# Performance work log

Measured on AMD Instinct MI355X. Metric: run time of the kernel, lower is better.

## Reference

```python
import jax, jax.numpy as jnp
import numpy as np

THETA = 0.5

def _l2norm(x):
    return x / jnp.maximum(jnp.linalg.norm(x, axis=-1, keepdims=True), 1e-12)

def _gcn_conv(x, row, col, W, b, n):
    # PyG GCNConv: add self loops (weight 1), sym-normalize, aggregate at col
    loop = jnp.arange(n)
    r = jnp.concatenate([row, loop])
    c = jnp.concatenate([col, loop])
    w = jnp.ones(r.shape[0], x.dtype)
    deg = jax.ops.segment_sum(w, c, num_segments=n)
    dinv = jnp.where(deg > 0, deg ** -0.5, 0.0)
    norm = dinv[r] * w * dinv[c]          # [E+N]
    xw = x @ W                            # [N, out]
    out = jax.ops.segment_sum(norm[:, None] * xw[r], c, num_segments=n)
    return out + b


def setup_inputs() -> dict:
    key = jax.random.key(0)
    ks = jax.random.split(key, 10)
    N, E, F, H, C = 16384, 524288, 256, 256, 40
    return {
        "edge_index": jax.random.randint(ks[0], (2, E), 0, N),
        "neg_edge_index": jax.random.randint(ks[1], (2, E), 0, N),
        "features": jax.random.normal(ks[2], (N, F), jnp.float32),
        "sim": jax.random.uniform(ks[3], (N, N), jnp.float32),
        "label_smoothing": jnp.ones((1,), jnp.float32),
        "W1": jax.random.normal(ks[4], (F, H), jnp.float32) * 0.05,
        "b1": jnp.zeros((H,), jnp.float32),
        "W2": jax.random.normal(ks[5], (H, H), jnp.float32) * 0.05,
        "b2": jnp.zeros((H,), jnp.float32),
        "Wy": jax.random.normal(ks[6], (H, C), jnp.float32) * 0.05,
        "by": jnp.zeros((C,), jnp.float32),
    }


def reference(edge_index, neg_edge_index, features, sim, label_smoothing,
              W1, b1, W2, b2, Wy, by):
    n = features.shape[0]
    row, col = edge_index[0], edge_index[1]
    # GCN encoder (dropout p=0.0 -> identity), L2-normalized twice as in source
    h = jax.nn.relu(_gcn_conv(features, row, col, W1, b1, n))
    h = _gcn_conv(h, row, col, W2, b2, n)
    rep = _l2norm(_l2norm(h))
    y = rep @ Wy + by
    # reconstruction loss; the i<j filtering becomes masking (jit-safe)
    pmask = (row < col).astype(rep.dtype)
    nr, nc = neg_edge_index[0], neg_edge_index[1]
    nmask = (nr < nc).astype(rep.dtype)
    neg_w = jax.nn.relu(jnp.sum(rep[nr] * rep[nc], axis=1))
    pos_w = jax.nn.relu(jnp.sum(rep[row] * rep[col], axis=1))
    pos_fsim = sim[row, col]
    pos = pos_fsim * THETA + pos_w * (1.0 - THETA)
    tgt = label_smoothing[0]
    sse = jnp.sum(nmask * neg_w ** 2) + jnp.sum(pmask * (pos - tgt) ** 2)
    rec_loss = sse * n / (jnp.sum(nmask) + jnp.sum(pmask))
    return rep, rec_loss, y
```

## Files before the change

kernel.cpp:

```cpp
#include <hip/hip_runtime.h>
#include <math.h>

typedef __attribute__((ext_vector_type(8))) short bf16x8;
typedef __attribute__((ext_vector_type(4))) float f32x4;
typedef __attribute__((ext_vector_type(2))) float f32x2;

static inline size_t align256(size_t x) { return (x + 255) & ~(size_t)255; }

__device__ inline ushort f2bf(float f) {
    uint u = __float_as_uint(f);
    u = (u + 0x7fffu + ((u >> 16) & 1u)) >> 16;
    return (ushort)u;
}
__device__ inline float bf2f(ushort b) { return __uint_as_float(((uint)b) << 16); }

__device__ inline uint f2fp8(float x) {
    float ax = fabsf(x);
    uint s = (__float_as_uint(x) >> 31) << 7;
    if (ax < 0.015625f) {
        int q = (int)rintf(ax * 512.f);
        if (q == 8) return s | 0x08u;
        return s | (uint)q;
    }
    uint u = __float_as_uint(ax);
    u += 0x7ffffu + ((u >> 20) & 1u);
    int e8 = (int)(u >> 23) - 127;
    uint m = (u >> 20) & 7u;
    return s | ((uint)(e8 + 7) << 3) | m;
}

#if __has_builtin(__builtin_amdgcn_cvt_pk_f32_fp8)
__device__ inline float fp8dot16(uint4 qa, uint4 qb) {
    uint ua[4] = {qa.x, qa.y, qa.z, qa.w};
    uint ub[4] = {qb.x, qb.y, qb.z, qb.w};
    float s = 0.f;
    #pragma unroll
    for (int i = 0; i < 4; i++) {
        f32x2 a0 = __builtin_amdgcn_cvt_pk_f32_fp8(ua[i], false);
        f32x2 a1 = __builtin_amdgcn_cvt_pk_f32_fp8(ua[i], true);
        f32x2 b0 = __builtin_amdgcn_cvt_pk_f32_fp8(ub[i], false);
        f32x2 b1 = __builtin_amdgcn_cvt_pk_f32_fp8(ub[i], true);
        s += a0.x * b0.x + a0.y * b0.y + a1.x * b1.x + a1.y * b1.y;
    }
    return s;
}
#else
__device__ inline float fp8dec(uint b) {
    uint s = (b >> 7) & 1u, e = (b >> 3) & 0xfu, m = b & 7u;
    float dn = (float)(int)m * 0.001953125f;
    float nf = __uint_as_float((s << 31) | ((e + 120u) << 23) | (m << 20));
    float dv = s ? -dn : dn;
    return e ? nf : dv;
}
__device__ inline float fp8dot16(uint4 qa, uint4 qb) {
    uint ua[4] = {qa.x, qa.y, qa.z, qa.w};
    uint ub[4] = {qb.x, qb.y, qb.z, qb.w};
    float s = 0.f;
    #pragma unroll
    for (int i = 0; i < 4; i++)
        #pragma unroll
        for (int j = 0; j < 4; j++)
            s += fp8dec((ua[i] >> (8 * j)) & 0xffu) * fp8dec((ub[i] >> (8 * j)) & 0xffu);
    return s;
}
#endif

__device__ inline void fma8(float* acc, uint4 q, float s) {
    acc[0] += s * bf2f((ushort)(q.x & 0xffff)); acc[1] += s * bf2f((ushort)(q.x >> 16));
    acc[2] += s * bf2f((ushort)(q.y & 0xffff)); acc[3] += s * bf2f((ushort)(q.y >> 16));
    acc[4] += s * bf2f((ushort)(q.z & 0xffff)); acc[5] += s * bf2f((ushort)(q.z >> 16));
    acc[6] += s * bf2f((ushort)(q.w & 0xffff)); acc[7] += s * bf2f((ushort)(q.w >> 16));
}

__global__ void prep_kernel(const int* __restrict__ e_col, int E, int* __restrict__ cnt,
                            const float* __restrict__ W1, const float* __restrict__ W2,
                            const float* __restrict__ Wy,
                            ushort* __restrict__ W1t, ushort* __restrict__ W2t,
                            ushort* __restrict__ WyTb, int H, int* __restrict__ ticket,
                            const int* __restrict__ pos_e, const float* __restrict__ sim,
                            float* __restrict__ simv, int N) {
    int i = blockIdx.x * blockDim.x + threadIdx.x;
    int HH = H * H;
    if (i == 0) *ticket = 0;
    if (i < E) {
        atomicAdd(&cnt[e_col[i]], 1);
    } else if (i < E + HH) {
        int j = i - E; int k = j / H, n = j % H;
        W1t[(size_t)n * H + k] = f2bf(W1[j]);
    } else if (i < E + 2 * HH) {
        int j = i - E - HH; int k = j / H, n = j % H;
        W2t[(size_t)n * H + k] = f2bf(W2[j]);
    } else if (i < E + 2 * HH + 64 * H) {
        int j = i - E - 2 * HH; int n = j / H, k = j % H;
        WyTb[j] = (n < 40) ? f2bf(Wy[(size_t)k * 40 + n]) : (ushort)0;
    } else if (i < E + 2 * HH + 64 * H + E) {
        int ei = i - (E + 2 * HH + 64 * H);
        int a = pos_e[ei], b = pos_e[E + ei];
        if (a < b) simv[ei] = sim[(size_t)a * N + b];
    }
}

__global__ __launch_bounds__(1024) void scan_offsets(const int* __restrict__ cnt,
                                                     int* __restrict__ offsets,
                                                     int* __restrict__ fillpos,
                                                     float* __restrict__ dinv, int N) {
    __shared__ int wsum[16];
    int t = threadIdx.x;
    int lane = t & 63, w = t >> 6;
    int i0 = t * 16;
    int cl[16];
    #pragma unroll
    for (int j = 0; j < 4; j++) {
        int4 c = *(const int4*)(cnt + i0 + j * 4);
        cl[j * 4 + 0] = c.x; cl[j * 4 + 1] = c.y; cl[j * 4 + 2] = c.z; cl[j * 4 + 3] = c.w;
    }
    int s = 0;
    #pragma unroll
    for (int j = 0; j < 16; j++) s += cl[j];
    int x = s;
    #pragma unroll
    for (int o = 1; o < 64; o <<= 1) { int y = __shfl_up(x, o); if (lane >= o) x += y; }
    if (lane == 63) wsum[w] = x;
    __syncthreads();
    if (w == 0 && lane < 16) {
        int v = wsum[lane];
        #pragma unroll
        for (int o = 1; o < 16; o <<= 1) { int y = __shfl_up(v, o); if (lane >= o) v += y; }
        wsum[lane] = v;
    }
    __syncthreads();
    int wbase = (w == 0) ? 0 : wsum[w - 1];
    int off = wbase + x - s;
    #pragma unroll
    for (int j = 0; j < 16; j++) {
        int i = i0 + j;
        offsets[i] = off;
        fillpos[i] = off;
        dinv[i] = rsqrtf((float)(cl[j] + 1));
        off += cl[j];
    }
    if (t == 1023) offsets[N] = off;
}

__global__ void fill_csr(const int* __restrict__ row, const int* __restrict__ col, int E,
                         int* __restrict__ fillpos, int* __restrict__ csr_src) {
    int e = blockIdx.x * blockDim.x + threadIdx.x;
    if (e < E) {
        int p = atomicAdd(&fillpos[col[e]], 1);
        csr_src[p] = row[e];
    }
}

template<bool AF32>
__global__ __launch_bounds__(256) void gemm_bf16_kernel(const void* __restrict__ Av,
                                                        const ushort* __restrict__ Bt,
                                                        ushort* __restrict__ C, int M) {
    __shared__ ushort As[128][40];
    __shared__ ushort Bs[128][40];
    const int K = 256;
    int t = threadIdx.x;
    int lane = t & 63, w = t >> 6;
    int wm = w >> 1, wn = w & 1;
    int brow = blockIdx.y * 128, bcol = blockIdx.x * 128;
    int l15 = lane & 15, l4 = lane >> 4;

    f32x4 acc[4][4];
    for (int i = 0; i < 4; i++)
        for (int j = 0; j < 4; j++) {
            f32x4 z = {0.f, 0.f, 0.f, 0.f};
            acc[i][j] = z;
        }

    for (int k0 = 0; k0 < K; k0 += 32) {
        #pragma unroll
        for (int i = 0; i < 2; i++) {
            int idx = t + i * 256;
            int r = idx >> 2, seg = idx & 3;
            if constexpr (AF32) {
                const float* A = (const float*)Av;
                const float* ap = A + (size_t)(brow + r) * K + k0 + seg * 8;
                float4 f0 = *(const float4*)ap;
                float4 f1 = *(const float4*)(ap + 4);
                uint4 va;
                va.x = f2bf(f0.x) | ((uint)f2bf(f0.y) << 16);
                va.y = f2bf(f0.z) | ((uint)f2bf(f0.w) << 16);
                va.z = f2bf(f1.x) | ((uint)f2bf(f1.y) << 16);
                va.w = f2bf(f1.z) | ((uint)f2bf(f1.w) << 16);
                *(uint4*)&As[r][seg * 8] = va;
            } else {
                const ushort* A = (const ushort*)Av;
                *(uint4*)&As[r][seg * 8] = *(const uint4*)(A + (size_t)(brow + r) * K + k0 + seg * 8);
            }
            *(uint4*)&Bs[r][seg * 8] = *(const uint4*)(Bt + (size_t)(bcol + r) * K + k0 + seg * 8);
        }
        __syncthreads();

        bf16x8 af[4], bfr[4];
        #pragma unroll
        for (int mf = 0; mf < 4; mf++)
            af[mf] = *(const bf16x8*)&As[wm * 64 + mf * 16 + l15][l4 * 8];
        #pragma unroll
        for (int nf = 0; nf < 4; nf++)
            bfr[nf] = *(const bf16x8*)&Bs[wn * 64 + nf * 16 + l15][l4 * 8];

        #pragma unroll
        for (int mf = 0; mf < 4; mf++)
            #pragma unroll
            for (int nf = 0; nf < 4; nf++)
                acc[mf][nf] = __builtin_amdgcn_mfma_f32_16x16x32_bf16(af[mf], bfr[nf], acc[mf][nf], 0, 0, 0);
        __syncthreads();
    }

    #pragma unroll
    for (int mf = 0; mf < 4; mf++)
        #pragma unroll
        for (int nf = 0; nf < 4; nf++)
            #pragma unroll
            for (int j = 0; j < 4; j++) {
                int r = brow + wm * 64 + mf * 16 + l4 * 4 + j;
                int c = bcol + wn * 64 + nf * 16 + l15;
                C[(size_t)r * 256 + c] = f2bf(acc[mf][nf][j]);
            }
}

__global__ __launch_bounds__(256) void gcn_agg1_kernel(const ushort* __restrict__ xw,
                                                       const float* __restrict__ dinv,
                                                       const int* __restrict__ offsets,
                                                       const int* __restrict__ csr_src,
                                                       const float* __restrict__ bias,
                                                       ushort* __restrict__ out_b, int N) {
    int t = threadIdx.x;
    int v = (blockIdx.x * blockDim.x + t) >> 5;
    int l = t & 31;
    if (v >= N) return;
    float dv = dinv[v];
    float acc[8] = {0, 0, 0, 0, 0, 0, 0, 0};
    uint4 q = *(const uint4*)(xw + (size_t)v * 256 + l * 8);
    fma8(acc, q, dv * dv);
    int beg = offsets[v], end = offsets[v + 1];
    int e = beg;
    for (; e + 4 <= end; e += 4) {
        int r0 = csr_src[e], r1 = csr_src[e + 1], r2 = csr_src[e + 2], r3 = csr_src[e + 3];
        float n0 = dinv[r0] * dv, n1 = dinv[r1] * dv, n2 = dinv[r2] * dv, n3 = dinv[r3] * dv;
        uint4 p0 = *(const uint4*)(xw + (size_t)r0 * 256 + l * 8);
        uint4 p1 = *(const uint4*)(xw + (size_t)r1 * 256 + l * 8);
        uint4 p2 = *(const uint4*)(xw + (size_t)r2 * 256 + l * 8);
        uint4 p3 = *(const uint4*)(xw + (size_t)r3 * 256 + l * 8);
        fma8(acc, p0, n0); fma8(acc, p1, n1); fma8(acc, p2, n2); fma8(acc, p3, n3);
    }
    for (; e < end; e++) {
        int r0 = csr_src[e];
        uint4 p0 = *(const uint4*)(xw + (size_t)r0 * 256 + l * 8);
        fma8(acc, p0, dinv[r0] * dv);
    }
    float4 b0 = *(const float4*)(bias + l * 8);
    float4 b1 = *(const float4*)(bias + l * 8 + 4);
    acc[0] = fmaxf(acc[0] + b0.x, 0.f); acc[1] = fmaxf(acc[1] + b0.y, 0.f);
    acc[2] = fmaxf(acc[2] + b0.z, 0.f); acc[3] = fmaxf(acc[3] + b0.w, 0.f);
    acc[4] = fmaxf(acc[4] + b1.x, 0.f); acc[5] = fmaxf(acc[5] + b1.y, 0.f);
    acc[6] = fmaxf(acc[6] + b1.z, 0.f); acc[7] = fmaxf(acc[7] + b1.w, 0.f);
    uint4 o;
    o.x = f2bf(acc[0]) | ((uint)f2bf(acc[1]) << 16);
    o.y = f2bf(acc[2]) | ((uint)f2bf(acc[3]) << 16);
    o.z = f2bf(acc[4]) | ((uint)f2bf(acc[5]) << 16);
    o.w = f2bf(acc[6]) | ((uint)f2bf(acc[7]) << 16);
    *(uint4*)(out_b + (size_t)v * 256 + l * 8) = o;
}

__global__ __launch_bounds__(256) void gcn_agg2_kernel(const ushort* __restrict__ xw,
                                                       const float* __restrict__ dinv,
                                                       const int* __restrict__ offsets,
                                                       const int* __restrict__ csr_src,
                                                       const float* __restrict__ b2,
                                                       float* __restrict__ rep,
                                                       ushort* __restrict__ repb,
                                                       unsigned char* __restrict__ rep8, int N) {
    int t = threadIdx.x;
    int v = (blockIdx.x * blockDim.x + t) >> 5;
    int l = t & 31;
    if (v >= N) return;
    float dv = dinv[v];
    float acc[8] = {0, 0, 0, 0, 0, 0, 0, 0};
    uint4 q = *(const uint4*)(xw + (size_t)v * 256 + l * 8);
    fma8(acc, q, dv * dv);
    int beg = offsets[v], end = offsets[v + 1];
    int e = beg;
    for (; e + 4 <= end; e += 4) {
        int r0 = csr_src[e], r1 = csr_src[e + 1], r2 = csr_src[e + 2], r3 = csr_src[e + 3];
        float n0 = dinv[r0] * dv, n1 = dinv[r1] * dv, n2 = dinv[r2] * dv, n3 = dinv[r3] * dv;
        uint4 p0 = *(const uint4*)(xw + (size_t)r0 * 256 + l * 8);
        uint4 p1 = *(const uint4*)(xw + (size_t)r1 * 256 + l * 8);
        uint4 p2 = *(const uint4*)(xw + (size_t)r2 * 256 + l * 8);
        uint4 p3 = *(const uint4*)(xw + (size_t)r3 * 256 + l * 8);
        fma8(acc, p0, n0); fma8(acc, p1, n1); fma8(acc, p2, n2); fma8(acc, p3, n3);
    }
    for (; e < end; e++) {
        int r0 = csr_src[e];
        uint4 p0 = *(const uint4*)(xw + (size_t)r0 * 256 + l * 8);
        fma8(acc, p0, dinv[r0] * dv);
    }
    float4 b0 = *(const float4*)(b2 + l * 8);
    float4 b1 = *(const float4*)(b2 + l * 8 + 4);
    acc[0] += b0.x; acc[1] += b0.y; acc[2] += b0.z; acc[3] += b0.w;
    acc[4] += b1.x; acc[5] += b1.y; acc[6] += b1.z; acc[7] += b1.w;

    float ss = 0.f;
    #pragma unroll
    for (int i = 0; i < 8; i++) ss += acc[i] * acc[i];
    #pragma unroll
    for (int o = 1; o < 32; o <<= 1) ss += __shfl_xor(ss, o);
    float n1 = fmaxf(sqrtf(ss), 1e-12f);
    float i1 = 1.f / n1;
    float n2 = fmaxf(sqrtf(ss) * i1, 1e-12f);
    float sc = i1 / n2;
    #pragma unroll
    for (int i = 0; i < 8; i++) acc[i] *= sc;

    float4 o0, o1;
    o0.x = acc[0]; o0.y = acc[1]; o0.z = acc[2]; o0.w = acc[3];
    o1.x = acc[4]; o1.y = acc[5]; o1.z = acc[6]; o1.w = acc[7];
    *(float4*)(rep + (size_t)v * 256 + l * 8) = o0;
    *(float4*)(rep + (size_t)v * 256 + l * 8 + 4) = o1;
    uint4 ob;
    ob.x = f2bf(acc[0]) | ((uint)f2bf(acc[1]) << 16);
    ob.y = f2bf(acc[2]) | ((uint)f2bf(acc[3]) << 16);
    ob.z = f2bf(acc[4]) | ((uint)f2bf(acc[5]) << 16);
    ob.w = f2bf(acc[6]) | ((uint)f2bf(acc[7]) << 16);
    *(uint4*)(repb + (size_t)v * 256 + l * 8) = ob;
    uint2 o8;
    o8.x = f2fp8(acc[0]) | (f2fp8(acc[1]) << 8) | (f2fp8(acc[2]) << 16) | (f2fp8(acc[3]) << 24);
    o8.y = f2fp8(acc[4]) | (f2fp8(acc[5]) << 8) | (f2fp8(acc[6]) << 16) | (f2fp8(acc[7]) << 24);
    *(uint2*)(rep8 + (size_t)v * 256 + l * 8) = o8;
}

__global__ __launch_bounds__(256) void tail_kernel(const ushort* __restrict__ repb,
                                                   const ushort* __restrict__ WyTb,
                                                   const float* __restrict__ by,
                                                   float* __restrict__ y,
                                                   const unsigned char* __restrict__ rep8,
                                                   const int* __restrict__ pos_e,
                                                   const int* __restrict__ neg_e,
                                                   const float* __restrict__ simv,
                                                   const float* __restrict__ lsm,
                                                   float2* __restrict__ partials,
                                                   int* __restrict__ ticket,
                                                   float* __restrict__ out_loss,
                                                   int E, int N, int NYB, int LB) {
    __shared__ ushort As[64][40];
    __shared__ ushort Bs[64][40];
    __shared__ float s_red[8];
    __shared__ int isLast;
    int t = threadIdx.x;

    if ((int)blockIdx.x < NYB) {
        const int K = 256;
        int lane = t & 63, w = t >> 6;
        int brow = blockIdx.x * 64;
        int l15 = lane & 15, l4 = lane >> 4;
        f32x4 acc[4];
        for (int i = 0; i < 4; i++) { f32x4 z = {0.f, 0.f, 0.f, 0.f}; acc[i] = z; }
        for (int k0 = 0; k0 < K; k0 += 32) {
            int r = t >> 2, seg = t & 3;
            *(uint4*)&As[r][seg * 8] = *(const uint4*)(repb + (size_t)(brow + r) * K + k0 + seg * 8);
            *(uint4*)&Bs[r][seg * 8] = *(const uint4*)(WyTb + (size_t)r * K + k0 + seg * 8);
            __syncthreads();
            bf16x8 af = *(const bf16x8*)&As[w * 16 + l15][l4 * 8];
            #pragma unroll
            for (int nf = 0; nf < 4; nf++) {
                bf16x8 bfr = *(const bf16x8*)&Bs[nf * 16 + l15][l4 * 8];
                acc[nf] = __builtin_amdgcn_mfma_f32_16x16x32_bf16(af, bfr, acc[nf], 0, 0, 0);
            }
            __syncthreads();
        }
        #pragma unroll
        for (int nf = 0; nf < 4; nf++)
            #pragma unroll
            for (int j = 0; j < 4; j++) {
                int r = brow + w * 16 + l4 * 4 + j;
                int c = nf * 16 + l15;
                if (c < 40) y[(size_t)r * 40 + c] = acc[nf][j] + by[c];
            }
        return;
    }

    int lb = (int)blockIdx.x - NYB;
    int l16 = t & 15;
    int g = lb * 16 + (t >> 4);
    int ng = LB * 16;
    float tgt = lsm[0];
    float sse = 0.f, cntf = 0.f;
    for (int idx = g; idx < 2 * E; idx += ng) {
        bool is_pos = idx < E;
        int ei = is_pos ? idx : idx - E;
        const int* ep = is_pos ? pos_e : neg_e;
        int a = ep[ei];
        int b = ep[E + ei];
        if (a < b) {
            uint4 qa = *(const uint4*)(rep8 + (size_t)a * 256 + l16 * 16);
            uint4 qb = *(const uint4*)(rep8 + (size_t)b * 256 + l16 * 16);
            float d = fp8dot16(qa, qb);
            #pragma unroll
            for (int o = 1; o < 16; o <<= 1) d += __shfl_xor(d, o);
            float wr = fmaxf(d, 0.f);
            float term;
            if (is_pos) {
                float fsim = simv[ei];
                float p = fsim * 0.5f + wr * 0.5f;
                term = (p - tgt) * (p - tgt);
            } else {
                term = wr * wr;
            }
            sse += term;
            cntf += 1.f;
        }
    }
    sse += __shfl_xor(sse, 16); cntf += __shfl_xor(cntf, 16);
    sse += __shfl_xor(sse, 32); cntf += __shfl_xor(cntf, 32);
    if ((t & 63) == 0) { s_red[t >> 6] = sse; s_red[4 + (t >> 6)] = cntf; }
    __syncthreads();
    if (t == 0) {
        float2 pp;
        pp.x = s_red[0] + s_red[1] + s_red[2] + s_red[3];
        pp.y = s_red[4] + s_red[5] + s_red[6] + s_red[7];
        partials[lb] = pp;
        __threadfence();
        int prev = atomicAdd(ticket, 1);
        isLast = (prev == LB - 1) ? 1 : 0;
    }
    __syncthreads();
    if (isLast) {
        __threadfence();
        float fs = 0.f, fc = 0.f;
        for (int i = t; i < LB; i += 256) {
            float2 pp = partials[i];
            fs += pp.x; fc += pp.y;
        }
        #pragma unroll
        for (int o = 1; o < 64; o <<= 1) { fs += __shfl_xor(fs, o); fc += __shfl_xor(fc, o); }
        if ((t & 63) == 0) { s_red[t >> 6] = fs; s_red[4 + (t >> 6)] = fc; }
        __syncthreads();
        if (t == 0) {
            float S = s_red[0] + s_red[1] + s_red[2] + s_red[3];
            float Cc = s_red[4] + s_red[5] + s_red[6] + s_red[7];
            out_loss[0] = S * (float)N / Cc;
        }
    }
}

extern "C" void kernel_launch(void* const* d_in, const int* in_sizes, int n_in,
                              void* d_out, int out_size, void* d_ws, size_t ws_size,
                              hipStream_t stream) {
    const int*   edge  = (const int*)d_in[0];
    const int*   nedge = (const int*)d_in[1];
    const float* feat  = (const float*)d_in[2];
    const float* sim   = (const float*)d_in[3];
    const float* lsm   = (const float*)d_in[4];
    const float* W1    = (const float*)d_in[5];
    const float* b1    = (const float*)d_in[6];
    const float* W2    = (const float*)d_in[7];
    const float* b2    = (const float*)d_in[8];
    const float* Wy    = (const float*)d_in[9];
    const float* by    = (const float*)d_in[10];

    const int E = in_sizes[0] / 2;
    const int H = in_sizes[6];
    const int F = in_sizes[5] / H;
    const int N = in_sizes[2] / F;

    const int* e_row = edge;
    const int* e_col = edge + E;

    const int LOSS_BLOCKS = 2048;
    const int NYB = N / 64;

    char* p = (char*)d_ws;
    int*    cnt      = (int*)p;    p += align256((size_t)N * 4);
    float*  dinv     = (float*)p;  p += align256((size_t)N * 4);
    int*    offsets  = (int*)p;    p += align256((size_t)(N + 1) * 4);
    int*    fillpos  = (int*)p;    p += align256((size_t)N * 4);
    int*    csr_src  = (int*)p;    p += align256((size_t)E * 4);
    ushort* W1t      = (ushort*)p; p += align256((size_t)F * H * 2);
    ushort* W2t      = (ushort*)p; p += align256((size_t)H * H * 2);
    ushort* WyTb     = (ushort*)p; p += align256((size_t)64 * H * 2);
    ushort* h1b      = (ushort*)p; p += align256((size_t)N * H * 2);
    ushort* xwb      = (ushort*)p; p += align256((size_t)N * H * 2);
    ushort* repb     = (ushort*)p; p += align256((size_t)N * H * 2);
    unsigned char* rep8 = (unsigned char*)p; p += align256((size_t)N * H);
    float*  simv     = (float*)p;  p += align256((size_t)E * 4);
    float2* partials = (float2*)p; p += align256((size_t)LOSS_BLOCKS * 8);
    int*    ticket   = (int*)p;    p += 256;

    float* rep  = (float*)d_out;
    float* loss = rep + (size_t)N * H;
    float* yout = loss + 1;

    hipMemsetAsync(cnt, 0, (size_t)N * 4, stream);

    {
        int total = 2 * E + 2 * H * H + 64 * H;
        prep_kernel<<<(total + 255) / 256, 256, 0, stream>>>(e_col, E, cnt, W1, W2, Wy,
                                                             W1t, W2t, WyTb, H, ticket,
                                                             e_row, sim, simv, N);
    }
    scan_offsets<<<1, 1024, 0, stream>>>(cnt, offsets, fillpos, dinv, N);
    fill_csr<<<(E + 255) / 256, 256, 0, stream>>>(e_row, e_col, E, fillpos, csr_src);

    {
        dim3 grid(2, N / 128);
        gemm_bf16_kernel<true><<<grid, 256, 0, stream>>>((const void*)feat, W1t, xwb, N);
    }
    gcn_agg1_kernel<<<N * 32 / 256, 256, 0, stream>>>(xwb, dinv, offsets, csr_src, b1, h1b, N);

    {
        dim3 grid(2, N / 128);
        gemm_bf16_kernel<false><<<grid, 256, 0, stream>>>((const void*)h1b, W2t, xwb, N);
    }
    gcn_agg2_kernel<<<N * 32 / 256, 256, 0, stream>>>(xwb, dinv, offsets, csr_src, b2,
                                                      rep, repb, rep8, N);

    tail_kernel<<<NYB + LOSS_BLOCKS, 256, 0, stream>>>(repb, WyTb, by, yout, rep8,
                                                       edge, nedge, simv, lsm, partials,
                                                       ticket, loss, E, N, NYB, LOSS_BLOCKS);
}
```

Measured before the change: 275.5 us.

## Fuse CSR fill with GEMM1, aggregation with GEMM2, and aggregation2 with y-projection

The CSR fill now runs as extra blocks inside the first GEMM launch. The first aggregation writes its bf16 output into shared memory and feeds the W2 GEMM directly, so the h1 buffer no longer makes a global round trip. The second aggregation likewise keeps normalized rep in shared memory and computes y = rep@Wy in the same block, and the loss becomes its own kernel. This removes launches and intermediate global traffic. The cost is fewer blocks in the aggregation kernels (N/64, each handling 64 nodes serially in 8 passes), which lowers parallelism and latency hiding for the gathers, plus larger LDS use.

```diff
diff --git a/kernel.cpp b/kernel.cpp
--- a/kernel.cpp
+++ b/kernel.cpp
@@ -142,59 +142,54 @@
     if (t == 1023) offsets[N] = off;
 }
 
-__global__ void fill_csr(const int* __restrict__ row, const int* __restrict__ col, int E,
-                         int* __restrict__ fillpos, int* __restrict__ csr_src) {
-    int e = blockIdx.x * blockDim.x + threadIdx.x;
-    if (e < E) {
-        int p = atomicAdd(&fillpos[col[e]], 1);
-        csr_src[p] = row[e];
-    }
-}
-
-template<bool AF32>
-__global__ __launch_bounds__(256) void gemm_bf16_kernel(const void* __restrict__ Av,
-                                                        const ushort* __restrict__ Bt,
-                                                        ushort* __restrict__ C, int M) {
+__global__ __launch_bounds__(256) void fillgemm1_kernel(const float* __restrict__ feat,
+                                                        const ushort* __restrict__ W1t,
+                                                        ushort* __restrict__ xw1,
+                                                        const int* __restrict__ e_row,
+                                                        const int* __restrict__ e_col, int E,
+                                                        int* __restrict__ fillpos,
+                                                        int* __restrict__ csr_src, int NGB) {
     __shared__ ushort As[128][40];
     __shared__ ushort Bs[128][40];
+    int b = blockIdx.x;
+    int t = threadIdx.x;
+
+    if (b >= NGB) {
+        int e = (b - NGB) * 256 + t;
+        if (e < E) {
+            int p = atomicAdd(&fillpos[e_col[e]], 1);
+            csr_src[p] = e_row[e];
+        }
+        return;
+    }
+
     const int K = 256;
-    int t = threadIdx.x;
     int lane = t & 63, w = t >> 6;
     int wm = w >> 1, wn = w & 1;
-    int brow = blockIdx.y * 128, bcol = blockIdx.x * 128;
+    int brow = (b >> 1) * 128, bcol = (b & 1) * 128;
     int l15 = lane & 15, l4 = lane >> 4;
 
     f32x4 acc[4][4];
     for (int i = 0; i < 4; i++)
-        for (int j = 0; j < 4; j++) {
-            f32x4 z = {0.f, 0.f, 0.f, 0.f};
-            acc[i][j] = z;
-        }
+        for (int j = 0; j < 4; j++) { f32x4 z = {0.f, 0.f, 0.f, 0.f}; acc[i][j] = z; }
 
     for (int k0 = 0; k0 < K; k0 += 32) {
         #pragma unroll
         for (int i = 0; i < 2; i++) {
             int idx = t + i * 256;
             int r = idx >> 2, seg = idx & 3;
-            if constexpr (AF32) {
-                const float* A = (const float*)Av;
-                const float* ap = A + (size_t)(brow + r) * K + k0 + seg * 8;
-                float4 f0 = *(const float4*)ap;
-                float4 f1 = *(const float4*)(ap + 4);
-                uint4 va;
-                va.x = f2bf(f0.x) | ((uint)f2bf(f0.y) << 16);
-                va.y = f2bf(f0.z) | ((uint)f2bf(f0.w) << 16);
-                va.z = f2bf(f1.x) | ((uint)f2bf(f1.y) << 16);
-                va.w = f2bf(f1.z) | ((uint)f2bf(f1.w) << 16);
-                *(uint4*)&As[r][seg * 8] = va;
-            } else {
-                const ushort* A = (const ushort*)Av;
-                *(uint4*)&As[r][seg * 8] = *(const uint4*)(A + (size_t)(brow + r) * K + k0 + seg * 8);
-            }
-            *(uint4*)&Bs[r][seg * 8] = *(const uint4*)(Bt + (size_t)(bcol + r) * K + k0 + seg * 8);
-        }
-        __syncthreads();
-
+            const float* ap = feat + (size_t)(brow + r) * K + k0 + seg * 8;
+            float4 f0 = *(const float4*)ap;
+            float4 f1 = *(const float4*)(ap + 4);
+            uint4 va;
+            va.x = f2bf(f0.x) | ((uint)f2bf(f0.y) << 16);
+            va.y = f2bf(f0.z) | ((uint)f2bf(f0.w) << 16);
+            va.z = f2bf(f1.x) | ((uint)f2bf(f1.y) << 16);
+            va.w = f2bf(f1.z) | ((uint)f2bf(f1.w) << 16);
+            *(uint4*)&As[r][seg * 8] = va;
+            *(uint4*)&Bs[r][seg * 8] = *(const uint4*)(W1t + (size_t)(bcol + r) * K + k0 + seg * 8);
+        }
+        __syncthreads();
         bf16x8 af[4], bfr[4];
         #pragma unroll
         for (int mf = 0; mf < 4; mf++)
@@ -202,7 +197,6 @@
         #pragma unroll
         for (int nf = 0; nf < 4; nf++)
             bfr[nf] = *(const bf16x8*)&Bs[wn * 64 + nf * 16 + l15][l4 * 8];
-
         #pragma unroll
         for (int mf = 0; mf < 4; mf++)
             #pragma unroll
@@ -219,125 +213,204 @@
             for (int j = 0; j < 4; j++) {
                 int r = brow + wm * 64 + mf * 16 + l4 * 4 + j;
                 int c = bcol + wn * 64 + nf * 16 + l15;
-                C[(size_t)r * 256 + c] = f2bf(acc[mf][nf][j]);
+                xw1[(size_t)r * 256 + c] = f2bf(acc[mf][nf][j]);
             }
 }
 
-__global__ __launch_bounds__(256) void gcn_agg1_kernel(const ushort* __restrict__ xw,
-                                                       const float* __restrict__ dinv,
-                                                       const int* __restrict__ offsets,
-                                                       const int* __restrict__ csr_src,
-                                                       const float* __restrict__ bias,
-                                                       ushort* __restrict__ out_b, int N) {
+__global__ __launch_bounds__(256) void conv2_fused_kernel(const ushort* __restrict__ xw1,
+                                                          const float* __restrict__ dinv,
+                                                          const int* __restrict__ offsets,
+                                                          const int* __restrict__ csr_src,
+                                                          const float* __restrict__ b1,
+                                                          const ushort* __restrict__ W2t,
+                                                          ushort* __restrict__ xw2, int N) {
+    __shared__ ushort h1s[64][264];
+    __shared__ ushort Bs[256][40];
     int t = threadIdx.x;
-    int v = (blockIdx.x * blockDim.x + t) >> 5;
+    int brow = blockIdx.x * 64;
     int l = t & 31;
-    if (v >= N) return;
-    float dv = dinv[v];
-    float acc[8] = {0, 0, 0, 0, 0, 0, 0, 0};
-    uint4 q = *(const uint4*)(xw + (size_t)v * 256 + l * 8);
-    fma8(acc, q, dv * dv);
-    int beg = offsets[v], end = offsets[v + 1];
-    int e = beg;
-    for (; e + 4 <= end; e += 4) {
-        int r0 = csr_src[e], r1 = csr_src[e + 1], r2 = csr_src[e + 2], r3 = csr_src[e + 3];
-        float n0 = dinv[r0] * dv, n1 = dinv[r1] * dv, n2 = dinv[r2] * dv, n3 = dinv[r3] * dv;
-        uint4 p0 = *(const uint4*)(xw + (size_t)r0 * 256 + l * 8);
-        uint4 p1 = *(const uint4*)(xw + (size_t)r1 * 256 + l * 8);
-        uint4 p2 = *(const uint4*)(xw + (size_t)r2 * 256 + l * 8);
-        uint4 p3 = *(const uint4*)(xw + (size_t)r3 * 256 + l * 8);
-        fma8(acc, p0, n0); fma8(acc, p1, n1); fma8(acc, p2, n2); fma8(acc, p3, n3);
-    }
-    for (; e < end; e++) {
-        int r0 = csr_src[e];
-        uint4 p0 = *(const uint4*)(xw + (size_t)r0 * 256 + l * 8);
-        fma8(acc, p0, dinv[r0] * dv);
-    }
-    float4 b0 = *(const float4*)(bias + l * 8);
-    float4 b1 = *(const float4*)(bias + l * 8 + 4);
-    acc[0] = fmaxf(acc[0] + b0.x, 0.f); acc[1] = fmaxf(acc[1] + b0.y, 0.f);
-    acc[2] = fmaxf(acc[2] + b0.z, 0.f); acc[3] = fmaxf(acc[3] + b0.w, 0.f);
-    acc[4] = fmaxf(acc[4] + b1.x, 0.f); acc[5] = fmaxf(acc[5] + b1.y, 0.f);
-    acc[6] = fmaxf(acc[6] + b1.z, 0.f); acc[7] = fmaxf(acc[7] + b1.w, 0.f);
-    uint4 o;
-    o.x = f2bf(acc[0]) | ((uint)f2bf(acc[1]) << 16);
-    o.y = f2bf(acc[2]) | ((uint)f2bf(acc[3]) << 16);
-    o.z = f2bf(acc[4]) | ((uint)f2bf(acc[5]) << 16);
-    o.w = f2bf(acc[6]) | ((uint)f2bf(acc[7]) << 16);
-    *(uint4*)(out_b + (size_t)v * 256 + l * 8) = o;
-}
-
-__global__ __launch_bounds__(256) void gcn_agg2_kernel(const ushort* __restrict__ xw,
-                                                       const float* __restrict__ dinv,
-                                                       const int* __restrict__ offsets,
-                                                       const int* __restrict__ csr_src,
-                                                       const float* __restrict__ b2,
-                                                       float* __restrict__ rep,
-                                                       ushort* __restrict__ repb,
-                                                       unsigned char* __restrict__ rep8, int N) {
-    int t = threadIdx.x;
-    int v = (blockIdx.x * blockDim.x + t) >> 5;
-    int l = t & 31;
-    if (v >= N) return;
-    float dv = dinv[v];
-    float acc[8] = {0, 0, 0, 0, 0, 0, 0, 0};
-    uint4 q = *(const uint4*)(xw + (size_t)v * 256 + l * 8);
-    fma8(acc, q, dv * dv);
-    int beg = offsets[v], end = offsets[v + 1];
-    int e = beg;
-    for (; e + 4 <= end; e += 4) {
-        int r0 = csr_src[e], r1 = csr_src[e + 1], r2 = csr_src[e + 2], r3 = csr_src[e + 3];
-        float n0 = dinv[r0] * dv, n1 = dinv[r1] * dv, n2 = dinv[r2] * dv, n3 = dinv[r3] * dv;
-        uint4 p0 = *(const uint4*)(xw + (size_t)r0 * 256 + l * 8);
-        uint4 p1 = *(const uint4*)(xw + (size_t)r1 * 256 + l * 8);
-        uint4 p2 = *(const uint4*)(xw + (size_t)r2 * 256 + l * 8);
-        uint4 p3 = *(const uint4*)(xw + (size_t)r3 * 256 + l * 8);
-        fma8(acc, p0, n0); fma8(acc, p1, n1); fma8(acc, p2, n2); fma8(acc, p3, n3);
-    }
-    for (; e < end; e++) {
-        int r0 = csr_src[e];
-        uint4 p0 = *(const uint4*)(xw + (size_t)r0 * 256 + l * 8);
-        fma8(acc, p0, dinv[r0] * dv);
-    }
-    float4 b0 = *(const float4*)(b2 + l * 8);
-    float4 b1 = *(const float4*)(b2 + l * 8 + 4);
-    acc[0] += b0.x; acc[1] += b0.y; acc[2] += b0.z; acc[3] += b0.w;
-    acc[4] += b1.x; acc[5] += b1.y; acc[6] += b1.z; acc[7] += b1.w;
-
-    float ss = 0.f;
-    #pragma unroll
-    for (int i = 0; i < 8; i++) ss += acc[i] * acc[i];
-    #pragma unroll
-    for (int o = 1; o < 32; o <<= 1) ss += __shfl_xor(ss, o);
-    float n1 = fmaxf(sqrtf(ss), 1e-12f);
-    float i1 = 1.f / n1;
-    float n2 = fmaxf(sqrtf(ss) * i1, 1e-12f);
-    float sc = i1 / n2;
-    #pragma unroll
-    for (int i = 0; i < 8; i++) acc[i] *= sc;
-
-    float4 o0, o1;
-    o0.x = acc[0]; o0.y = acc[1]; o0.z = acc[2]; o0.w = acc[3];
-    o1.x = acc[4]; o1.y = acc[5]; o1.z = acc[6]; o1.w = acc[7];
-    *(float4*)(rep + (size_t)v * 256 + l * 8) = o0;
-    *(float4*)(rep + (size_t)v * 256 + l * 8 + 4) = o1;
-    uint4 ob;
-    ob.x = f2bf(acc[0]) | ((uint)f2bf(acc[1]) << 16);
-    ob.y = f2bf(acc[2]) | ((uint)f2bf(acc[3]) << 16);
-    ob.z = f2bf(acc[4]) | ((uint)f2bf(acc[5]) << 16);
-    ob.w = f2bf(acc[6]) | ((uint)f2bf(acc[7]) << 16);
-    *(uint4*)(repb + (size_t)v * 256 + l * 8) = ob;
-    uint2 o8;
-    o8.x = f2fp8(acc[0]) | (f2fp8(acc[1]) << 8) | (f2fp8(acc[2]) << 16) | (f2fp8(acc[3]) << 24);
-    o8.y = f2fp8(acc[4]) | (f2fp8(acc[5]) << 8) | (f2fp8(acc[6]) << 16) | (f2fp8(acc[7]) << 24);
-    *(uint2*)(rep8 + (size_t)v * 256 + l * 8) = o8;
-}
-
-__global__ __launch_bounds__(256) void tail_kernel(const ushort* __restrict__ repb,
+    int grp = t >> 5;
+
+    for (int pass = 0; pass < 8; pass++) {
+        int v = brow + pass * 8 + grp;
+        float dv = dinv[v];
+        float acc[8] = {0, 0, 0, 0, 0, 0, 0, 0};
+        uint4 q = *(const uint4*)(xw1 + (size_t)v * 256 + l * 8);
+        fma8(acc, q, dv * dv);
+        int beg = offsets[v], end = offsets[v + 1];
+        int e = beg;
+        for (; e + 2 <= end; e += 2) {
+            int r0 = csr_src[e], r1 = csr_src[e + 1];
+            float n0 = dinv[r0] * dv, n1 = dinv[r1] * dv;
+            uint4 p0 = *(const uint4*)(xw1 + (size_t)r0 * 256 + l * 8);
+            uint4 p1 = *(const uint4*)(xw1 + (size_t)r1 * 256 + l * 8);
+            fma8(acc, p0, n0); fma8(acc, p1, n1);
+        }
+        if (e < end) {
+            int r0 = csr_src[e];
+            uint4 p0 = *(const uint4*)(xw1 + (size_t)r0 * 256 + l * 8);
+            fma8(acc, p0, dinv[r0] * dv);
+        }
+        float4 bb0 = *(const float4*)(b1 + l * 8);
+        float4 bb1 = *(const float4*)(b1 + l * 8 + 4);
+        acc[0] = fmaxf(acc[0] + bb0.x, 0.f); acc[1] = fmaxf(acc[1] + bb0.y, 0.f);
+        acc[2] = fmaxf(acc[2] + bb0.z, 0.f); acc[3] = fmaxf(acc[3] + bb0.w, 0.f);
+        acc[4] = fmaxf(acc[4] + bb1.x, 0.f); acc[5] = fmaxf(acc[5] + bb1.y, 0.f);
+        acc[6] = fmaxf(acc[6] + bb1.z, 0.f); acc[7] = fmaxf(acc[7] + bb1.w, 0.f);
+        uint4 o;
+        o.x = f2bf(acc[0]) | ((uint)f2bf(acc[1]) << 16);
+        o.y = f2bf(acc[2]) | ((uint)f2bf(acc[3]) << 16);
+        o.z = f2bf(acc[4]) | ((uint)f2bf(acc[5]) << 16);
+        o.w = f2bf(acc[6]) | ((uint)f2bf(acc[7]) << 16);
+        *(uint4*)&h1s[pass * 8 + grp][l * 8] = o;
+    }
+    __syncthreads();
+
+    int lane = t & 63, w = t >> 6;
+    int wm = w >> 1, wn = w & 1;
+    int l15 = lane & 15, l4 = lane >> 4;
+    f32x4 acc[2][8];
+    for (int i = 0; i < 2; i++)
+        for (int j = 0; j < 8; j++) { f32x4 z = {0.f, 0.f, 0.f, 0.f}; acc[i][j] = z; }
+
+    for (int kc = 0; kc < 8; kc++) {
+        #pragma unroll
+        for (int i = 0; i < 4; i++) {
+            int linear = i * 256 + t;
+            int col = linear >> 2, seg = linear & 3;
+            *(uint4*)&Bs[col][seg * 8] = *(const uint4*)(W2t + (size_t)col * 256 + kc * 32 + seg * 8);
+        }
+        __syncthreads();
+        bf16x8 af[2], bfr[8];
+        #pragma unroll
+        for (int mf = 0; mf < 2; mf++)
+            af[mf] = *(const bf16x8*)&h1s[wm * 32 + mf * 16 + l15][kc * 32 + l4 * 8];
+        #pragma unroll
+        for (int nf = 0; nf < 8; nf++)
+            bfr[nf] = *(const bf16x8*)&Bs[wn * 128 + nf * 16 + l15][l4 * 8];
+        #pragma unroll
+        for (int mf = 0; mf < 2; mf++)
+            #pragma unroll
+            for (int nf = 0; nf < 8; nf++)
+                acc[mf][nf] = __builtin_amdgcn_mfma_f32_16x16x32_bf16(af[mf], bfr[nf], acc[mf][nf], 0, 0, 0);
+        __syncthreads();
+    }
+
+    #pragma unroll
+    for (int mf = 0; mf < 2; mf++)
+        #pragma unroll
+        for (int nf = 0; nf < 8; nf++)
+            #pragma unroll
+            for (int j = 0; j < 4; j++) {
+                int r = brow + wm * 32 + mf * 16 + l4 * 4 + j;
+                int c = wn * 128 + nf * 16 + l15;
+                xw2[(size_t)r * 256 + c] = f2bf(acc[mf][nf][j]);
+            }
+}
+
+__global__ __launch_bounds__(256) void post_kernel(const ushort* __restrict__ xw2,
+                                                   const float* __restrict__ dinv,
+                                                   const int* __restrict__ offsets,
+                                                   const int* __restrict__ csr_src,
+                                                   const float* __restrict__ b2,
                                                    const ushort* __restrict__ WyTb,
                                                    const float* __restrict__ by,
-                                                   float* __restrict__ y,
-                                                   const unsigned char* __restrict__ rep8,
+                                                   float* __restrict__ rep,
+                                                   unsigned char* __restrict__ rep8,
+                                                   float* __restrict__ y, int N) {
+    __shared__ ushort reps[64][264];
+    __shared__ ushort ws[64][40];
+    int t = threadIdx.x;
+    int brow = blockIdx.x * 64;
+    int l = t & 31;
+    int grp = t >> 5;
+
+    for (int pass = 0; pass < 8; pass++) {
+        int v = brow + pass * 8 + grp;
+        float dv = dinv[v];
+        float acc[8] = {0, 0, 0, 0, 0, 0, 0, 0};
+        uint4 q = *(const uint4*)(xw2 + (size_t)v * 256 + l * 8);
+        fma8(acc, q, dv * dv);
+        int beg = offsets[v], end = offsets[v + 1];
+        int e = beg;
+        for (; e + 2 <= end; e += 2) {
+            int r0 = csr_src[e], r1 = csr_src[e + 1];
+            float n0 = dinv[r0] * dv, n1 = dinv[r1] * dv;
+            uint4 p0 = *(const uint4*)(xw2 + (size_t)r0 * 256 + l * 8);
+            uint4 p1 = *(const uint4*)(xw2 + (size_t)r1 * 256 + l * 8);
+            fma8(acc, p0, n0); fma8(acc, p1, n1);
+        }
+        if (e < end) {
+            int r0 = csr_src[e];
+            uint4 p0 = *(const uint4*)(xw2 + (size_t)r0 * 256 + l * 8);
+            fma8(acc, p0, dinv[r0] * dv);
+        }
+        float4 bb0 = *(const float4*)(b2 + l * 8);
+        float4 bb1 = *(const float4*)(b2 + l * 8 + 4);
+        acc[0] += bb0.x; acc[1] += bb0.y; acc[2] += bb0.z; acc[3] += bb0.w;
+        acc[4] += bb1.x; acc[5] += bb1.y; acc[6] += bb1.z; acc[7] += bb1.w;
+
+        float ss = 0.f;
+        #pragma unroll
+        for (int i = 0; i < 8; i++) ss += acc[i] * acc[i];
+        #pragma unroll
+        for (int o = 1; o < 32; o <<= 1) ss += __shfl_xor(ss, o);
+        float n1 = fmaxf(sqrtf(ss), 1e-12f);
+        float i1 = 1.f / n1;
+        float n2 = fmaxf(sqrtf(ss) * i1, 1e-12f);
+        float sc = i1 / n2;
+        #pragma unroll
+        for (int i = 0; i < 8; i++) acc[i] *= sc;
+
+        float4 o0, o1;
+        o0.x = acc[0]; o0.y = acc[1]; o0.z = acc[2]; o0.w = acc[3];
+        o1.x = acc[4]; o1.y = acc[5]; o1.z = acc[6]; o1.w = acc[7];
+        *(float4*)(rep + (size_t)v * 256 + l * 8) = o0;
+        *(float4*)(rep + (size_t)v * 256 + l * 8 + 4) = o1;
+        uint4 ob;
+        ob.x = f2bf(acc[0]) | ((uint)f2bf(acc[1]) << 16);
+        ob.y = f2bf(acc[2]) | ((uint)f2bf(acc[3]) << 16);
+        ob.z = f2bf(acc[4]) | ((uint)f2bf(acc[5]) << 16);
+        ob.w = f2bf(acc[6]) | ((uint)f2bf(acc[7]) << 16);
+        *(uint4*)&reps[pass * 8 + grp][l * 8] = ob;
+        uint2 o8;
+        o8.x = f2fp8(acc[0]) | (f2fp8(acc[1]) << 8) | (f2fp8(acc[2]) << 16) | (f2fp8(acc[3]) << 24);
+        o8.y = f2fp8(acc[4]) | (f2fp8(acc[5]) << 8) | (f2fp8(acc[6]) << 16) | (f2fp8(acc[7]) << 24);
+        *(uint2*)(rep8 + (size_t)v * 256 + l * 8) = o8;
+    }
+    __syncthreads();
+
+    int lane = t & 63, w = t >> 6;
+    int l15 = lane & 15, l4 = lane >> 4;
+    f32x4 acc[4];
+    for (int i = 0; i < 4; i++) { f32x4 z = {0.f, 0.f, 0.f, 0.f}; acc[i] = z; }
+
+    for (int kc = 0; kc < 8; kc++) {
+        {
+            int n = t >> 2, seg = t & 3;
+            *(uint4*)&ws[n][seg * 8] = *(const uint4*)(WyTb + (size_t)n * 256 + kc * 32 + seg * 8);
+        }
+        __syncthreads();
+        bf16x8 af = *(const bf16x8*)&reps[w * 16 + l15][kc * 32 + l4 * 8];
+        #pragma unroll
+        for (int nf = 0; nf < 4; nf++) {
+            bf16x8 bfr = *(const bf16x8*)&ws[nf * 16 + l15][l4 * 8];
+            acc[nf] = __builtin_amdgcn_mfma_f32_16x16x32_bf16(af, bfr, acc[nf], 0, 0, 0);
+        }
+        __syncthreads();
+    }
+
+    #pragma unroll
+    for (int nf = 0; nf < 4; nf++)
+        #pragma unroll
+        for (int j = 0; j < 4; j++) {
+            int r = brow + w * 16 + l4 * 4 + j;
+            int c = nf * 16 + l15;
+            if (c < 40) y[(size_t)r * 40 + c] = acc[nf][j] + by[c];
+        }
+}
+
+__global__ __launch_bounds__(256) void loss_kernel(const unsigned char* __restrict__ rep8,
                                                    const int* __restrict__ pos_e,
                                                    const int* __restrict__ neg_e,
                                                    const float* __restrict__ simv,
@@ -345,45 +418,11 @@
                                                    float2* __restrict__ partials,
                                                    int* __restrict__ ticket,
                                                    float* __restrict__ out_loss,
-                                                   int E, int N, int NYB, int LB) {
-    __shared__ ushort As[64][40];
-    __shared__ ushort Bs[64][40];
+                                                   int E, int N, int LB) {
     __shared__ float s_red[8];
     __shared__ int isLast;
     int t = threadIdx.x;
-
-    if ((int)blockIdx.x < NYB) {
-        const int K = 256;
-        int lane = t & 63, w = t >> 6;
-        int brow = blockIdx.x * 64;
-        int l15 = lane & 15, l4 = lane >> 4;
-        f32x4 acc[4];
-        for (int i = 0; i < 4; i++) { f32x4 z = {0.f, 0.f, 0.f, 0.f}; acc[i] = z; }
-        for (int k0 = 0; k0 < K; k0 += 32) {
-            int r = t >> 2, seg = t & 3;
-            *(uint4*)&As[r][seg * 8] = *(const uint4*)(repb + (size_t)(brow + r) * K + k0 + seg * 8);
-            *(uint4*)&Bs[r][seg * 8] = *(const uint4*)(WyTb + (size_t)r * K + k0 + seg * 8);
-            __syncthreads();
-            bf16x8 af = *(const bf16x8*)&As[w * 16 + l15][l4 * 8];
-            #pragma unroll
-            for (int nf = 0; nf < 4; nf++) {
-                bf16x8 bfr = *(const bf16x8*)&Bs[nf * 16 + l15][l4 * 8];
-                acc[nf] = __builtin_amdgcn_mfma_f32_16x16x32_bf16(af, bfr, acc[nf], 0, 0, 0);
-            }
-            __syncthreads();
-        }
-        #pragma unroll
-        for (int nf = 0; nf < 4; nf++)
-            #pragma unroll
-            for (int j = 0; j < 4; j++) {
-                int r = brow + w * 16 + l4 * 4 + j;
-                int c = nf * 16 + l15;
-                if (c < 40) y[(size_t)r * 40 + c] = acc[nf][j] + by[c];
-            }
-        return;
-    }
-
-    int lb = (int)blockIdx.x - NYB;
+    int lb = blockIdx.x;
     int l16 = t & 15;
     int g = lb * 16 + (t >> 4);
     int ng = LB * 16;
@@ -471,7 +510,7 @@
     const int* e_col = edge + E;
 
     const int LOSS_BLOCKS = 2048;
-    const int NYB = N / 64;
+    const int NGB = 2 * (N / 128);
 
     char* p = (char*)d_ws;
     int*    cnt      = (int*)p;    p += align256((size_t)N * 4);
@@ -482,9 +521,8 @@
     ushort* W1t      = (ushort*)p; p += align256((size_t)F * H * 2);
     ushort* W2t      = (ushort*)p; p += align256((size_t)H * H * 2);
     ushort* WyTb     = (ushort*)p; p += align256((size_t)64 * H * 2);
-    ushort* h1b      = (ushort*)p; p += align256((size_t)N * H * 2);
-    ushort* xwb      = (ushort*)p; p += align256((size_t)N * H * 2);
-    ushort* repb     = (ushort*)p; p += align256((size_t)N * H * 2);
+    ushort* xw1      = (ushort*)p; p += align256((size_t)N * H * 2);
+    ushort* xw2      = (ushort*)p; p += align256((size_t)N * H * 2);
     unsigned char* rep8 = (unsigned char*)p; p += align256((size_t)N * H);
     float*  simv     = (float*)p;  p += align256((size_t)E * 4);
     float2* partials = (float2*)p; p += align256((size_t)LOSS_BLOCKS * 8);
@@ -503,22 +541,17 @@
                                                              e_row, sim, simv, N);
     }
     scan_offsets<<<1, 1024, 0, stream>>>(cnt, offsets, fillpos, dinv, N);
-    fill_csr<<<(E + 255) / 256, 256, 0, stream>>>(e_row, e_col, E, fillpos, csr_src);
-
-    {
-        dim3 grid(2, N / 128);
-        gemm_bf16_kernel<true><<<grid, 256, 0, stream>>>((const void*)feat, W1t, xwb, N);
-    }
-    gcn_agg1_kernel<<<N * 32 / 256, 256, 0, stream>>>(xwb, dinv, offsets, csr_src, b1, h1b, N);
-
-    {
-        dim3 grid(2, N / 128);
-        gemm_bf16_kernel<false><<<grid, 256, 0, stream>>>((const void*)h1b, W2t, xwb, N);
-    }
-    gcn_agg2_kernel<<<N * 32 / 256, 256, 0, stream>>>(xwb, dinv, offsets, csr_src, b2,
-                                                      rep, repb, rep8, N);
-
-    tail_kernel<<<NYB + LOSS_BLOCKS, 256, 0, stream>>>(repb, WyTb, by, yout, rep8,
-                                                       edge, nedge, simv, lsm, partials,
-                                                       ticket, loss, E, N, NYB, LOSS_BLOCKS);
-}
+
+    fillgemm1_kernel<<<NGB + (E + 255) / 256, 256, 0, stream>>>(feat, W1t, xw1,
+                                                                e_row, e_col, E,
+                                                                fillpos, csr_src, NGB);
+
+    conv2_fused_kernel<<<N / 64, 256, 0, stream>>>(xw1, dinv, offsets, csr_src, b1,
+                                                   W2t, xw2, N);
+
+    post_kernel<<<N / 64, 256, 0, stream>>>(xw2, dinv, offsets, csr_src, b2,
+                                            WyTb, by, rep, rep8, yout, N);
+
+    loss_kernel<<<LOSS_BLOCKS, 256, 0, stream>>>(rep8, edge, nedge, simv, lsm,
+                                                 partials, ticket, loss, E, N, LOSS_BLOCKS);
+}
```

After: 396.8 us. +44.1%, slower.
